# Optimization experiments

Hardware: AMD Instinct MI355X
Metric: run time of the kernel (lower is better)

The kernel has to match this reference:

```python
import jax, jax.numpy as jnp
import numpy as np
import math

B, INST, C, HEADS, DH, CTX = 1, 4, 320, 8, 40, 768
FULL, HW = 512, 4096
SCALE = DH ** -0.5
EPS = 1e-5


def _ln(x, g, b):
    m = x.mean(-1, keepdims=True)
    v = ((x - m) ** 2).mean(-1, keepdims=True)
    return (x - m) / jnp.sqrt(v + EPS) * g + b


def _mha(x, ctx, Wq, Wk, Wv, Wo, bo, mask=None):
    # x: [b, n, C]; ctx: [b, m, ctx_dim]; mask: [b, n, m] bool (True = keep)
    b, n, _ = x.shape
    m = ctx.shape[1]
    q = (x @ Wq).reshape(b, n, HEADS, DH)
    k = (ctx @ Wk).reshape(b, m, HEADS, DH)
    v = (ctx @ Wv).reshape(b, m, HEADS, DH)
    sim = jnp.einsum('bihd,bjhd->bhij', q, k) * SCALE
    if mask is not None:
        sim = jnp.where(mask[:, None, :, :], sim, -jnp.finfo(sim.dtype).max)
    attn = jax.nn.softmax(sim, axis=-1)
    out = jnp.einsum('bhij,bjhd->bihd', attn, v).reshape(b, n, HEADS * DH)
    return out @ Wo + bo


def _fourier(x, num_freqs=8, temperature=100.0):
    freqs = temperature ** (jnp.arange(num_freqs, dtype=x.dtype) / num_freqs)
    parts = []
    for i in range(num_freqs):
        parts.append(jnp.sin(freqs[i] * x))
        parts.append(jnp.cos(freqs[i] * x))
    return jax.lax.stop_gradient(jnp.concatenate(parts, axis=-1))  # @torch.no_grad in source


def _resize(x, H, W):
    # torch F.interpolate bilinear, align_corners=False (half-pixel), no antialias
    return jax.image.resize(x, x.shape[:2] + (H, W), method='bilinear', antialias=False)


def setup_inputs() -> dict:
    key = jax.random.key(0)
    ks = jax.random.split(key, 32)
    s = 0.02
    inp = {
        'ca_x': jax.random.normal(ks[0], (B, INST + 1, HW, C), jnp.float32),
        'guidance_mask': jax.random.uniform(ks[1], (B, INST, FULL, FULL), jnp.float32),
        'supplement_mask': jax.random.uniform(ks[2], (B, 1, FULL, FULL), jnp.float32),
        'image_token': jax.random.normal(ks[3], (B, INST + 1, HW, C), jnp.float32),
        'context': jax.random.normal(ks[4], (INST + 1, 77, CTX), jnp.float32),
        'box': jax.random.uniform(ks[5], (B, INST, 8), jnp.float32),
        'img_features': jax.random.normal(ks[6], (B * INST, 257, CTX), jnp.float32),
        'bg_features': jax.random.normal(ks[7], (B, 257, CTX), jnp.float32),
        'sigmoid_values': jax.random.uniform(ks[8], (B, INST, FULL, FULL), jnp.float32),
        'Wq_obj': jax.random.normal(ks[9], (C, C), jnp.float32) * s,
        'Wk_obj': jax.random.normal(ks[10], (CTX, C), jnp.float32) * s,
        'Wv_obj': jax.random.normal(ks[11], (CTX, C), jnp.float32) * s,
        'Wo_obj': jax.random.normal(ks[12], (C, C), jnp.float32) * s,
        'bo_obj': jnp.zeros((C,), jnp.float32),
        'ln_g_obj': jnp.ones((C,), jnp.float32),
        'ln_b_obj': jnp.zeros((C,), jnp.float32),
        'Wq2': jax.random.normal(ks[13], (C, C), jnp.float32) * s,
        'Wk2': jax.random.normal(ks[14], (CTX, C), jnp.float32) * s,
        'Wv2': jax.random.normal(ks[15], (CTX, C), jnp.float32) * s,
        'Wo2': jax.random.normal(ks[16], (C, C), jnp.float32) * s,
        'bo2': jnp.zeros((C,), jnp.float32),
        'ln_g2': jnp.ones((C,), jnp.float32),
        'ln_b2': jnp.zeros((C,), jnp.float32),
        'pn_W1': jax.random.normal(ks[17], (128, 512), jnp.float32) * s,
        'pn_b1': jnp.zeros((512,), jnp.float32),
        'pn_W2': jax.random.normal(ks[18], (512, 512), jnp.float32) * s,
        'pn_b2': jnp.zeros((512,), jnp.float32),
        'pn_W3': jax.random.normal(ks[19], (512, CTX), jnp.float32) * s,
        'pn_b3': jnp.zeros((CTX,), jnp.float32),
        'la_Wq': jax.random.normal(ks[20], (C, C), jnp.float32) * s,
        'la_Wk': jax.random.normal(ks[21], (C, C), jnp.float32) * s,
        'la_Wv': jax.random.normal(ks[22], (C, C), jnp.float32) * s,
        'la_Wo': jax.random.normal(ks[23], (C, C), jnp.float32) * s,
        'la_bo': jnp.zeros((C,), jnp.float32),
        'height': FULL,
        'width': FULL,
    }
    return inp


def reference(ca_x, guidance_mask, supplement_mask, image_token, context, box,
              img_features, bg_features, sigmoid_values,
              Wq_obj, Wk_obj, Wv_obj, Wo_obj, bo_obj, ln_g_obj, ln_b_obj,
              Wq2, Wk2, Wv2, Wo2, bo2, ln_g2, ln_b2,
              pn_W1, pn_b1, pn_W2, pn_b2, pn_W3, pn_b3,
              la_Wq, la_Wk, la_Wv, la_Wo, la_bo,
              height, width):
    b, _, hw, c = ca_x.shape
    inst = guidance_mask.shape[1]
    down = int(math.sqrt(height * width // hw))
    H, W = height // down, width // down

    gm = _resize(guidance_mask, H, W)           # [B, inst, H, W]
    supp = _resize(supplement_mask, H, W)       # [B, 1, H, W]
    sig = _resize(sigmoid_values, H, W).reshape(b, inst, hw, 1)

    # PositionNet on boxes
    box_emb = _fourier(box.reshape(b * inst, 1, 8))          # [B*inst, 1, 128]
    h1 = jax.nn.silu(box_emb @ pn_W1 + pn_b1)
    h2 = jax.nn.silu(h1 @ pn_W2 + pn_b2)
    box_token = h2 @ pn_W3 + pn_b3                            # [B*inst, 1, 768]

    # foreground cross-attention (ea_obj)
    context_fg = jnp.concatenate([context[1:], img_features, box_token], axis=1)
    q_in = _ln(image_token[:, 1:].reshape(b * inst, hw, c), ln_g_obj, ln_b_obj)
    ea_x = _mha(q_in, context_fg, Wq_obj, Wk_obj, Wv_obj, Wo_obj, bo_obj)
    ea_x = ea_x.reshape(b, inst, hw, c) * sig

    ca_inst = ca_x[:, 1:] * sig + ea_x                        # [B, inst, HW, C]

    # background cross-attention (ea2)
    context_bg = jnp.concatenate([context[0:1], bg_features], axis=1)
    q2 = _ln(ca_inst.sum(axis=1).reshape(b, hw, c), ln_g2, ln_b2)
    ea_bg = _mha(q2, context_bg, Wq2, Wk2, Wv2, Wo2, bo2)     # [B, HW, C]
    ca0 = ca_x[:, 0] + ea_bg

    # layout self-attention with guidance-mask sparsity
    gm_all = jnp.concatenate([gm, supp], axis=1).reshape(b, inst + 1, hw)
    # sum over phases of outer products; clamp-to-1 in source only feeds the ==0 test
    sim_mask = jnp.einsum('bpi,bpj->bij', gm_all, gm_all) != 0  # [B, HW, HW] keep-mask
    fusion = _mha(image_token[:, 0], image_token[:, 0],
                  la_Wq, la_Wk, la_Wv, la_Wo, la_bo, mask=sim_mask)

    out = ca0 + ca_inst.sum(axis=1) + fusion                  # [B, HW, C]
    return out
```

## Files before the change

### kernel.cpp

```cpp
#include <hip/hip_runtime.h>
#include <hip/hip_bf16.h>
#include <math.h>

typedef unsigned short bhalf;
typedef unsigned int u32;
typedef unsigned long long u64;
typedef __attribute__((ext_vector_type(8))) short s16x8;
typedef __attribute__((ext_vector_type(4))) float f32x4;

#define SCALE_QK 0.15811388300841898f
#define K2E (SCALE_QK * 1.4426950408889634f)
#define NEG_INF (-3.402823466e38f)

__device__ __forceinline__ float bf2f(bhalf u){
    union { unsigned int i; float f; } v; v.i = ((unsigned int)u) << 16; return v.f;
}
__device__ __forceinline__ bhalf f2bf(float f){
    unsigned int x = __float_as_uint(f);
    unsigned int r = (x + 0x7fffu + ((x >> 16) & 1u)) >> 16;
    return (bhalf)r;
}
__device__ __forceinline__ float fexp2(float x){
    float r; asm("v_exp_f32 %0, %1" : "=v"(r) : "v"(x)); return r;
}
__device__ __forceinline__ u32 cvtpk(float lo, float hi){
    u32 r; asm("v_cvt_pk_bf16_f32 %0, %1, %2" : "=v"(r) : "v"(lo), "v"(hi)); return r;
}

struct WT12 { const float* in[12]; bhalf* out[12]; };

struct PrepArgs {
    const float *itok, *g_obj, *b_obj; bhalf *q_in, *x_la;
    WT12 wt;
    const float *gmask, *smask, *sgv; float *gm_all, *sig;
    const float *box, *W1, *b1, *W2, *b2, *W3, *b3; float* tok;
};

__global__ __launch_bounds__(320) void mega_prep(PrepArgs a){
    __shared__ float smem[64 * 65];
    const int bid = blockIdx.x, tid = threadIdx.x;
    if (bid < 16){
        float* emb = smem; float* h1 = smem + 128; float* h2 = smem + 640;
        const int bb = bid >> 2, sl = bid & 3;
        for (int t = tid; t < 128; t += 320){
            const int i = t >> 4, jj = t & 15, j = jj & 7;
            const float f = powf(100.f, (float)i * 0.125f);
            const float v = f * a.box[bb * 8 + j];
            emb[t] = (jj < 8) ? sinf(v) : cosf(v);
        }
        __syncthreads();
        for (int t = tid; t < 512; t += 320){
            float a0 = a.b1[t], a1 = 0.f, a2 = 0.f, a3 = 0.f;
#pragma unroll 8
            for (int k = 0; k < 32; ++k){
                a0 += emb[k]      * a.W1[k * 512 + t];
                a1 += emb[k + 32] * a.W1[(k + 32) * 512 + t];
                a2 += emb[k + 64] * a.W1[(k + 64) * 512 + t];
                a3 += emb[k + 96] * a.W1[(k + 96) * 512 + t];
            }
            const float x = (a0 + a1) + (a2 + a3);
            h1[t] = x / (1.f + __expf(-x));
        }
        __syncthreads();
        for (int t = tid; t < 512; t += 320){
            float a0 = a.b2[t], a1 = 0.f, a2 = 0.f, a3 = 0.f;
#pragma unroll 8
            for (int k = 0; k < 128; ++k){
                a0 += h1[k]       * a.W2[k * 512 + t];
                a1 += h1[k + 128] * a.W2[(k + 128) * 512 + t];
                a2 += h1[k + 256] * a.W2[(k + 256) * 512 + t];
                a3 += h1[k + 384] * a.W2[(k + 384) * 512 + t];
            }
            const float x = (a0 + a1) + (a2 + a3);
            h2[t] = x / (1.f + __expf(-x));
        }
        __syncthreads();
        if (tid < 192){
            const int t = sl * 192 + tid;
            float a0 = a.b3[t], a1 = 0.f, a2 = 0.f, a3 = 0.f;
#pragma unroll 8
            for (int k = 0; k < 128; ++k){
                a0 += h2[k]       * a.W3[k * 768 + t];
                a1 += h2[k + 128] * a.W3[(k + 128) * 768 + t];
                a2 += h2[k + 256] * a.W3[(k + 256) * 768 + t];
                a3 += h2[k + 384] * a.W3[(k + 384) * 768 + t];
            }
            a.tok[bb * 768 + t] = (a0 + a1) + (a2 + a3);
        }
    } else if (bid < 456){
        float (*T)[65] = (float(*)[65])smem;
        const int b = bid - 16;
        int w, t, K;
        if (b < 200){ w = b / 25; t = b % 25; K = 320; }
        else        { w = 8 + (b - 200) / 60; t = (b - 200) % 60; K = 768; }
        const int k0 = (t / 5) * 64, n0 = (t % 5) * 64;
        const float* in = a.wt.in[w];
        bhalf* out = a.wt.out[w];
        const int c = tid & 63, wv = tid >> 6;
        if (tid < 256){
#pragma unroll
            for (int r = 0; r < 16; ++r)
                T[wv + r * 4][c] = in[(long)(k0 + wv + r * 4) * 320 + n0 + c];
        }
        __syncthreads();
        if (tid < 256){
#pragma unroll
            for (int r = 0; r < 16; ++r)
                out[(long)(n0 + wv + r * 4) * K + k0 + c] = f2bf(T[c][wv + r * 4]);
        }
    } else if (bid < 600){
        if (tid < 256){
            const int b = bid - 456;
            const int p = b >> 4;
            const int i = (b & 15) * 256 + tid;
            const int y = i >> 6, x = i & 63;
            const int o = (8 * y + 3) * 512 + 8 * x + 3;
            const float* s; float* dst;
            if (p < 4){ s = a.gmask + (long)p * 262144; dst = a.gm_all + p * 4096; }
            else if (p == 4){ s = a.smask; dst = a.gm_all + 4 * 4096; }
            else { s = a.sgv + (long)(p - 5) * 262144; dst = a.sig + (p - 5) * 4096; }
            dst[i] = 0.25f * (s[o] + s[o + 1] + s[o + 512] + s[o + 513]);
        }
    } else {
        const int lane = tid & 63, wv = tid >> 6;
        const int wgid = (bid - 600) * 5 + wv;
        for (int row = wgid; row < 20480; row += 10240){
            if (row >= 16384){
                const int rr = row - 16384;
#pragma unroll
                for (int j = 0; j < 5; ++j){
                    const int c = lane + 64 * j;
                    a.x_la[(long)rr * 320 + c] = f2bf(a.itok[(long)rr * 320 + c]);
                }
                continue;
            }
            float v[5];
            float s = 0.f, sq = 0.f;
#pragma unroll
            for (int j = 0; j < 5; ++j){
                v[j] = a.itok[(long)(4096 + row) * 320 + lane + 64 * j];
                s += v[j]; sq += v[j] * v[j];
            }
#pragma unroll
            for (int o = 1; o < 64; o <<= 1){ s += __shfl_xor(s, o); sq += __shfl_xor(sq, o); }
            const float mean = s * (1.f / 320.f);
            const float var  = sq * (1.f / 320.f) - mean * mean;
            const float inv  = rsqrtf(var + 1e-5f);
#pragma unroll
            for (int j = 0; j < 5; ++j){
                const int c = lane + 64 * j;
                a.q_in[(long)row * 320 + c] = f2bf((v[j] - mean) * inv * a.g_obj[c] + a.b_obj[c]);
            }
        }
    }
}

__global__ __launch_bounds__(256) void mega_mask(
    const float* __restrict__ gm_all, u64* __restrict__ mb,
    const float* __restrict__ context, const float* __restrict__ imgf,
    const float* __restrict__ bgf, const float* __restrict__ boxtok, bhalf* __restrict__ out)
{
    __shared__ float smem[5440];
    const int tid = threadIdx.x;
    if (blockIdx.x < 256){
        const int r = blockIdx.x;
        const int i0 = (r & 63) << 6, j0 = (r >> 6) << 10;
        float* gi = smem;
        float* gj = smem + 320;
        for (int idx = tid; idx < 5 * 64; idx += 256)
            gi[idx] = gm_all[(idx >> 6) * 4096 + i0 + (idx & 63)];
        for (int idx = tid; idx < 5 * 1024; idx += 256)
            gj[idx] = gm_all[(idx >> 10) * 4096 + j0 + (idx & 1023)];
        __syncthreads();
        const int lane = tid & 63, wave = tid >> 6;
        const float a0 = gi[lane], a1 = gi[64 + lane], a2 = gi[128 + lane],
                    a3 = gi[192 + lane], a4 = gi[256 + lane];
        for (int ww = wave; ww < 16; ww += 4){
            u64 m = 0;
            for (int j = 0; j < 64; ++j){
                const int jj = (ww << 6) + j;
                const float dot = a0 * gj[jj] + a1 * gj[1024 + jj] + a2 * gj[2048 + jj]
                                + a3 * gj[3072 + jj] + a4 * gj[4096 + jj];
                m |= (u64)(dot != 0.f) << j;
            }
            mb[(long)((j0 >> 6) + ww) * 4096 + (i0 + lane)] = m;
        }
    } else {
        const int idx = (blockIdx.x - 256) * 256 + tid;
        const int i = idx / (336 * 768);
        const int r = (idx / 768) % 336;
        const int c = idx % 768;
        float v;
        if (i < 4){
            if (r < 77)       v = context[((long)(1 + i) * 77 + r) * 768 + c];
            else if (r < 334) v = imgf[((long)i * 257 + (r - 77)) * 768 + c];
            else if (r == 334) v = boxtok[i * 768 + c];
            else v = 0.f;
        } else {
            if (r < 77)       v = context[(long)r * 768 + c];
            else if (r < 334) v = bgf[(long)(r - 77) * 768 + c];
            else v = 0.f;
        }
        out[idx] = f2bf(v);
    }
}

template<int K>
__device__ __forceinline__ void gemm5x4_body(
    int bx, int by, const bhalf* __restrict__ A, const bhalf* __restrict__ Wt,
    bhalf* __restrict__ Cbf, int M, int kdm, float scale)
{
    const int wave = threadIdx.x >> 6, lane = threadIdx.x & 63;
    const int mb = bx * 256 + wave * 64;
    const int n0 = by * 64;
    const int klo = (lane >> 4) * 8;
    const bhalf* ap[4];
#pragma unroll
    for (int f = 0; f < 4; ++f){
        int mrow = mb + f * 16 + (lane & 15); if (mrow > M - 1) mrow = M - 1;
        ap[f] = A + (long)mrow * K + klo;
    }
    const bhalf* wp = Wt + (long)(n0 + (lane & 15)) * K + klo;
    const f32x4 fz = {0.f, 0.f, 0.f, 0.f};
    f32x4 acc[4][4];
#pragma unroll
    for (int f = 0; f < 4; ++f)
#pragma unroll
        for (int t = 0; t < 4; ++t) acc[f][t] = fz;
#pragma unroll
    for (int k0 = 0; k0 < K; k0 += 32){
        s16x8 av[4];
#pragma unroll
        for (int f = 0; f < 4; ++f) av[f] = *(const s16x8*)(ap[f] + k0);
        s16x8 bv[4];
#pragma unroll
        for (int t = 0; t < 4; ++t) bv[t] = *(const s16x8*)(wp + (long)t * 16 * K + k0);
#pragma unroll
        for (int f = 0; f < 4; ++f)
#pragma unroll
            for (int t = 0; t < 4; ++t)
                acc[f][t] = __builtin_amdgcn_mfma_f32_16x16x32_bf16(av[f], bv[t], acc[f][t], 0, 0, 0);
    }
#pragma unroll
    for (int f = 0; f < 4; ++f){
        const int rb = mb + f * 16 + ((threadIdx.x & 63) >> 4) * 4;
#pragma unroll
        for (int t = 0; t < 4; ++t){
            const int col = n0 + t * 16 + (threadIdx.x & 15);
            const int hh = col / 40, cc = col % 40;
#pragma unroll
            for (int r = 0; r < 4; ++r){
                const int row = rb + r;
                if (row >= M) continue;
                Cbf[(((long)(row / kdm) * 8 + hh) * kdm + (row % kdm)) * 40 + cc] = f2bf(acc[f][t][r] * scale);
            }
        }
    }
}

template<int K>
__device__ __forceinline__ void gemm_vt_body(
    int bx, int by, const bhalf* __restrict__ A, const bhalf* __restrict__ Wt,
    bhalf* __restrict__ Vt, int M, int vt_ns, int PAD, bhalf (*Tsh)[72])
{
    const int wave = threadIdx.x >> 6, lane = threadIdx.x & 63;
    const int m0 = bx * 64 + wave * 16;
    const int n0 = by * 64;
    int mrow = m0 + (lane & 15); if (mrow > M - 1) mrow = M - 1;
    const int klo = (lane >> 4) * 8;
    const bhalf* ap = A + (long)mrow * K + klo;
    const bhalf* wp = Wt + (long)(n0 + (lane & 15)) * K + klo;
    const f32x4 fz = {0.f, 0.f, 0.f, 0.f};
    f32x4 acc[4]; acc[0] = fz; acc[1] = fz; acc[2] = fz; acc[3] = fz;
#pragma unroll
    for (int k0 = 0; k0 < K; k0 += 32){
        s16x8 a = *(const s16x8*)(ap + k0);
#pragma unroll
        for (int t = 0; t < 4; ++t){
            s16x8 b = *(const s16x8*)(wp + (long)t * 16 * K + k0);
            acc[t] = __builtin_amdgcn_mfma_f32_16x16x32_bf16(a, b, acc[t], 0, 0, 0);
        }
    }
    const int hi = lane >> 4, l15 = lane & 15;
#pragma unroll
    for (int t = 0; t < 4; ++t)
#pragma unroll
        for (int r = 0; r < 4; ++r)
            Tsh[wave * 16 + hi * 4 + r][t * 16 + l15] = f2bf(acc[t][r]);
    __syncthreads();
    const int c = threadIdx.x & 63, jq = threadIdx.x >> 6;
    const int jbase = bx * 64 + jq * 16;
    if (jbase >= PAD) return;
    bhalf* vp = Vt + (long)(n0 + c) * vt_ns + jbase;
    if (jbase + 16 <= M){
        u32 wb[8];
#pragma unroll
        for (int p = 0; p < 8; ++p)
            wb[p] = (u32)Tsh[jq * 16 + 2 * p][c] | ((u32)Tsh[jq * 16 + 2 * p + 1][c] << 16);
        *(uint4*)vp       = make_uint4(wb[0], wb[1], wb[2], wb[3]);
        *(uint4*)(vp + 8) = make_uint4(wb[4], wb[5], wb[6], wb[7]);
    } else if (jbase >= M){
        *(uint4*)vp       = make_uint4(0, 0, 0, 0);
        *(uint4*)(vp + 8) = make_uint4(0, 0, 0, 0);
    } else {
        for (int jj = 0; jj < 16; ++jj)
            vp[jj] = (jbase + jj < M) ? Tsh[jq * 16 + jj][c] : (bhalf)0;
    }
}

struct ProjArgs {
    const bhalf *q_in, *ctx_all, *x_la;
    const bhalf *wqobjT, *wkobjT, *wk2T, *lawqT, *wvobjT, *wv2T, *lawvT;
    bhalf *q_obj, *k_obj, *k_bg, *qkl, *vt_obj, *vt_bg, *vt_l;
};

__global__ __launch_bounds__(256) void proj_packed(ProjArgs a){
    const int r = blockIdx.x;
    if (r < 320)       gemm5x4_body<320>(r % 64, r / 64, a.q_in, a.wqobjT, a.q_obj, 16384, 4096, K2E);
    else if (r < 480){ const int s = r - 320; const int by = s / 16, bx = s % 16;
        gemm5x4_body<320>(bx, by, a.x_la, a.lawqT, a.qkl, 4096, 4096, by < 5 ? K2E : 1.f); }
    else if (r < 510){ const int s = r - 480; gemm5x4_body<768>(s % 6, s / 6, a.ctx_all, a.wkobjT, a.k_obj, 1344, 336, 1.f); }
    else { const int s = r - 510; gemm5x4_body<768>(s % 2, s / 2, a.ctx_all + (size_t)4 * 336 * 768, a.wk2T, a.k_bg, 336, 336, 1.f); }
}

__global__ __launch_bounds__(256) void proj_vt(ProjArgs a){
    __shared__ bhalf Tsh[64][72];
    const int r = blockIdx.x;
    if (r < 150){ const int bz = r / 30, rem = r % 30;
        if (bz == 4) gemm_vt_body<768>(rem % 6, rem / 6, a.ctx_all + (size_t)4 * 336 * 768, a.wv2T, a.vt_bg, 336, 384, 384, Tsh);
        else gemm_vt_body<768>(rem % 6, rem / 6, a.ctx_all + (size_t)bz * 336 * 768, a.wvobjT, a.vt_obj + (size_t)bz * 320 * 384, 336, 384, 384, Tsh);
    }
    else { const int s = r - 150; gemm_vt_body<320>(s % 64, s / 64, a.x_la, a.lawvT, a.vt_l, 4096, 4096, 4096, Tsh); }
}

__global__ __launch_bounds__(256) void ln_rows_kernel(
    const float* __restrict__ in, const float* __restrict__ g, const float* __restrict__ b,
    bhalf* __restrict__ out)
{
    const int lane = threadIdx.x & 63;
    const int wgid = blockIdx.x * 4 + (threadIdx.x >> 6);
    for (int row = wgid; row < 4096; row += 4096){
        float v[5];
        float s = 0.f, sq = 0.f;
#pragma unroll
        for (int j = 0; j < 5; ++j){
            v[j] = in[(long)row * 320 + lane + 64 * j];
            s += v[j]; sq += v[j] * v[j];
        }
#pragma unroll
        for (int o = 1; o < 64; o <<= 1){ s += __shfl_xor(s, o); sq += __shfl_xor(sq, o); }
        const float mean = s * (1.f / 320.f);
        const float var  = sq * (1.f / 320.f) - mean * mean;
        const float inv  = rsqrtf(var + 1e-5f);
#pragma unroll
        for (int j = 0; j < 5; ++j){
            const int c = lane + 64 * j;
            out[(long)row * 320 + c] = f2bf((v[j] - mean) * inv * g[c] + b[c]);
        }
    }
}

template<int MODE>
__global__ __launch_bounds__(256) void gemm320(
    const bhalf* __restrict__ A, const bhalf* __restrict__ Wt,
    const float* __restrict__ bias, bhalf* __restrict__ Cbf,
    float* __restrict__ Cf, const float* __restrict__ add1, const float* __restrict__ add2,
    int M, int kdm, float ascale,
    const bhalf* __restrict__ A2, const bhalf* __restrict__ Wt2, const float* __restrict__ bias2)
{
    constexpr int K = 320;
    const int wave = threadIdx.x >> 6, lane = threadIdx.x & 63;
    const int m0 = blockIdx.x * 64 + wave * 16;
    const int n0 = blockIdx.y * 64;
    int mrow = m0 + (lane & 15); if (mrow > M - 1) mrow = M - 1;
    const int klo = (lane >> 4) * 8;
    const bhalf* ap = A + (long)mrow * K + klo;
    const bhalf* wp = Wt + (long)(n0 + (lane & 15)) * K + klo;
    const f32x4 fz = {0.f, 0.f, 0.f, 0.f};
    f32x4 acc[4]; acc[0] = fz; acc[1] = fz; acc[2] = fz; acc[3] = fz;
#pragma unroll
    for (int k0 = 0; k0 < K; k0 += 32){
        s16x8 a = *(const s16x8*)(ap + k0);
#pragma unroll
        for (int t = 0; t < 4; ++t){
            s16x8 b = *(const s16x8*)(wp + (long)t * 16 * K + k0);
            acc[t] = __builtin_amdgcn_mfma_f32_16x16x32_bf16(a, b, acc[t], 0, 0, 0);
        }
    }
    if (MODE == 6){
        const bhalf* ap2 = A2 + (long)mrow * K + klo;
        const bhalf* wp2 = Wt2 + (long)(n0 + (lane & 15)) * K + klo;
#pragma unroll
        for (int k0 = 0; k0 < K; k0 += 32){
            s16x8 a = *(const s16x8*)(ap2 + k0);
#pragma unroll
            for (int t = 0; t < 4; ++t){
                s16x8 b = *(const s16x8*)(wp2 + (long)t * 16 * K + k0);
                acc[t] = __builtin_amdgcn_mfma_f32_16x16x32_bf16(a, b, acc[t], 0, 0, 0);
            }
        }
    }
    if (MODE == 8){
#pragma unroll
        for (int i = 1; i < 4; ++i){
            const bhalf* api = A + (long)i * kdm + (long)mrow * K + klo;
#pragma unroll
            for (int k0 = 0; k0 < K; k0 += 32){
                s16x8 a = *(const s16x8*)(api + k0);
#pragma unroll
                for (int t = 0; t < 4; ++t){
                    s16x8 b = *(const s16x8*)(wp + (long)t * 16 * K + k0);
                    acc[t] = __builtin_amdgcn_mfma_f32_16x16x32_bf16(a, b, acc[t], 0, 0, 0);
                }
            }
        }
    }
    const int rb = m0 + (lane >> 4) * 4;
    int rin[4], rn[4];
    if (MODE == 5){
#pragma unroll
        for (int r = 0; r < 4; ++r){ const int row = rb + r; rin[r] = row / kdm; rn[r] = row % kdm; }
    }
#pragma unroll
    for (int t = 0; t < 4; ++t){
        const int col = n0 + t * 16 + (lane & 15);
        const int hh = col / 40, cc = col % 40;
#pragma unroll
        for (int r = 0; r < 4; ++r){
            const int row = rb + r;
            if (row >= M) continue;
            const float v = acc[t][r];
            if (MODE == 5)
                Cbf[(((long)rin[r] * 8 + hh) * kdm + rn[r]) * 40 + cc] = f2bf(v * ascale);
            else if (MODE == 6){
                const long o = (long)row * 320 + col;
                Cf[o] = v + bias[col] + bias2[col] + add1[o] + add2[o];
            }
            else if (MODE == 8){
                const long o = (long)row * 320 + col;
                float ssum = 0.f, cax = 0.f;
#pragma unroll
                for (int i = 0; i < 4; ++i){
                    const float sg = add2[i * 4096 + row];
                    ssum += sg;
                    cax += sg * add1[(long)i * 4096 * 320 + o];
                }
                Cf[o] = v + ssum * bias[col] + cax;
            }
        }
    }
}

template<bool GMM, bool PARTIAL, bool SIG>
__global__ __launch_bounds__(256) void flash4(
    const bhalf* __restrict__ Qh, const bhalf* __restrict__ Kh, const bhalf* __restrict__ Vt,
    bhalf* __restrict__ O, const u64* __restrict__ maskb,
    int NKV, long qh_is, long qh_hs, long kh_is, long kh_hs, long vt_is, int vt_ns, long o_is,
    const float* __restrict__ sigp, bhalf* __restrict__ pacc, float* __restrict__ pl)
{
    const int lane = threadIdx.x & 63, wave = threadIdx.x >> 6;
    const int l15 = lane & 15, hi = lane >> 4, klo = hi * 8;
    const int h = blockIdx.y;
    const int inst = PARTIAL ? 0 : blockIdx.z;
    const int g = PARTIAL ? blockIdx.z : 0;
    const int qbase = blockIdx.x * 256 + wave * 64;
    const s16x8 z8 = {0, 0, 0, 0, 0, 0, 0, 0};
    const f32x4 fz = {0.f, 0.f, 0.f, 0.f};

    s16x8 qa0[4], qa1[4];
#pragma unroll
    for (int qg = 0; qg < 4; ++qg){
        const bhalf* qp = Qh + inst * qh_is + h * qh_hs + (long)(qbase + qg * 16 + l15) * 40;
        qa0[qg] = *(const s16x8*)(qp + klo);
        qa1[qg] = (hi == 0) ? *(const s16x8*)(qp + 32) : z8;
    }
    const int krbase = 8 * (l15 >> 2) + (l15 & 3);
    const bhalf* khead = Kh + inst * kh_is + h * kh_hs;
    const bhalf* kbase = khead + (long)krbase * 40;

    const bhalf* vbase[3];
#pragma unroll
    for (int ct = 0; ct < 3; ++ct){
        int dr = h * 40 + ct * 16 + l15; if (dr > 319) dr = 319;
        vbase[ct] = Vt + inst * vt_is + (long)dr * vt_ns + hi * 8;
    }

    f32x4 acc[4][3];
    float l_run[4];
#pragma unroll
    for (int qg = 0; qg < 4; ++qg){
        acc[qg][0] = fz; acc[qg][1] = fz; acc[qg][2] = fz;
        l_run[qg] = 0.f;
    }

    auto soft_pv = [&](f32x4 (&d)[4], s16x8 (&vb)[3][2], float& lr, f32x4 (&ac)[3]){
        float csum = 0.f;
#pragma unroll
        for (int t = 0; t < 4; ++t)
#pragma unroll
            for (int r = 0; r < 4; ++r){
                const float p = fexp2(d[t][r]);
                d[t][r] = p; csum += p;
            }
        csum += __shfl_xor(csum, 16);
        csum += __shfl_xor(csum, 32);
        lr += csum;
#pragma unroll
        for (int s = 0; s < 2; ++s){
            union { u32 w[4]; s16x8 v; } pb;
            pb.w[0] = cvtpk(d[2 * s][0], d[2 * s][1]);
            pb.w[1] = cvtpk(d[2 * s][2], d[2 * s][3]);
            pb.w[2] = cvtpk(d[2 * s + 1][0], d[2 * s + 1][1]);
            pb.w[3] = cvtpk(d[2 * s + 1][2], d[2 * s + 1][3]);
#pragma unroll
            for (int ct = 0; ct < 3; ++ct)
                ac[ct] = __builtin_amdgcn_mfma_f32_16x16x32_bf16(vb[ct][s], pb.v, ac[ct], 0, 0, 0);
        }
    };

    const int ch0 = PARTIAL ? g * 8 : 0;
    const int chN = PARTIAL ? ch0 + 8 : (NKV >> 6);
    for (int ch = ch0; ch < chN; ++ch){
        const int c0 = ch << 6;
        s16x8 k0[4], k1[4];
#pragma unroll
        for (int t = 0; t < 4; ++t){
            const int toff = ((t >> 1) << 5) + ((t & 1) << 2);
            const bhalf* kp = kbase + (long)(c0 + toff) * 40;
            k0[t] = *(const s16x8*)(kp + klo);
            k1[t] = (hi == 0) ? *(const s16x8*)(kp + 32) : z8;
        }
        s16x8 vb[3][2];
#pragma unroll
        for (int ct = 0; ct < 3; ++ct)
#pragma unroll
            for (int s = 0; s < 2; ++s)
                vb[ct][s] = *(const s16x8*)(vbase[ct] + c0 + 32 * s);
        u64 M[4];
        if (GMM){
#pragma unroll
            for (int qg = 0; qg < 4; ++qg)
                M[qg] = maskb[(long)ch * 4096 + qbase + qg * 16 + l15];
        }
#pragma unroll
        for (int qg = 0; qg < 4; ++qg){
            f32x4 d[4];
#pragma unroll
            for (int t = 0; t < 4; ++t){
                d[t] = __builtin_amdgcn_mfma_f32_16x16x32_bf16(k0[t], qa0[qg], fz, 0, 0, 0);
                d[t] = __builtin_amdgcn_mfma_f32_16x16x32_bf16(k1[t], qa1[qg], d[t], 0, 0, 0);
            }
            if (GMM && !__all(M[qg] == ~0ull)){
                const u64 Mh = M[qg] >> (hi * 8);
#pragma unroll
                for (int t = 0; t < 4; ++t){
                    const int tb = ((t >> 1) << 5) + ((t & 1) << 2);
#pragma unroll
                    for (int r = 0; r < 4; ++r)
                        if (!((Mh >> (tb + r)) & 1)) d[t][r] = NEG_INF;
                }
            }
            soft_pv(d, vb, l_run[qg], acc[qg]);
        }
    }
    if (!PARTIAL && (NKV & 63)){
        const int c0 = (NKV >> 6) << 6;
        s16x8 k0[4], k1[4];
#pragma unroll
        for (int t = 0; t < 4; ++t){
            const int toff = ((t >> 1) << 5) + ((t & 1) << 2);
            int kr = c0 + toff + krbase; if (kr > NKV - 1) kr = NKV - 1;
            const bhalf* kp = khead + (long)kr * 40;
            k0[t] = *(const s16x8*)(kp + klo);
            k1[t] = (hi == 0) ? *(const s16x8*)(kp + 32) : z8;
        }
        s16x8 vb[3][2];
#pragma unroll
        for (int ct = 0; ct < 3; ++ct)
#pragma unroll
            for (int s = 0; s < 2; ++s)
                vb[ct][s] = *(const s16x8*)(vbase[ct] + c0 + 32 * s);
#pragma unroll
        for (int qg = 0; qg < 4; ++qg){
            f32x4 d[4];
#pragma unroll
            for (int t = 0; t < 4; ++t){
                d[t] = __builtin_amdgcn_mfma_f32_16x16x32_bf16(k0[t], qa0[qg], fz, 0, 0, 0);
                d[t] = __builtin_amdgcn_mfma_f32_16x16x32_bf16(k1[t], qa1[qg], d[t], 0, 0, 0);
            }
#pragma unroll
            for (int t = 0; t < 4; ++t){
                const int tb = ((t >> 1) << 5) + ((t & 1) << 2);
#pragma unroll
                for (int r = 0; r < 4; ++r)
                    if (c0 + tb + hi * 8 + r >= NKV) d[t][r] = NEG_INF;
            }
            soft_pv(d, vb, l_run[qg], acc[qg]);
        }
    }

    if (PARTIAL){
#pragma unroll
        for (int qg = 0; qg < 4; ++qg){
            const int q = qbase + qg * 16 + l15;
#pragma unroll
            for (int ct = 0; ct < 3; ++ct){
                bhalf* pb = pacc + ((((size_t)(g * 8 + h) * 3 + ct) * 4 + hi) * 4096 + q) * 4;
                uint2 w;
                w.x = cvtpk(acc[qg][ct][0], acc[qg][ct][1]);
                w.y = cvtpk(acc[qg][ct][2], acc[qg][ct][3]);
                *(uint2*)pb = w;
            }
            if (hi == 0)
                pl[(size_t)(g * 8 + h) * 4096 + q] = l_run[qg];
        }
    } else {
#pragma unroll
        for (int qg = 0; qg < 4; ++qg){
            const int q = qbase + qg * 16 + l15;
            float sc = 1.f / l_run[qg];
            if (SIG) sc *= sigp[(long)inst * 4096 + q];
            bhalf* op = O + inst * o_is + (long)q * 320 + h * 40;
#pragma unroll
            for (int ct = 0; ct < 3; ++ct){
                const int d0 = ct * 16 + hi * 4;
                if (d0 < 40){
                    uint2 w;
                    w.x = cvtpk(acc[qg][ct][0] * sc, acc[qg][ct][1] * sc);
                    w.y = cvtpk(acc[qg][ct][2] * sc, acc[qg][ct][3] * sc);
                    *(uint2*)(op + d0) = w;
                }
            }
        }
    }
}

__global__ __launch_bounds__(256) void combine_kernel(
    const bhalf* __restrict__ pacc, const float* __restrict__ pl, bhalf* __restrict__ O)
{
    const int idx = blockIdx.x * 256 + threadIdx.x;
    const int h = idx / (3 * 4096);
    const int r2 = idx % (3 * 4096);
    const int ct = r2 >> 12, q = r2 & 4095;
    float ls = 0.f;
#pragma unroll
    for (int g = 0; g < 8; ++g) ls += pl[(size_t)(g * 8 + h) * 4096 + q];
    float acc[16];
#pragma unroll
    for (int d = 0; d < 16; ++d) acc[d] = 0.f;
#pragma unroll
    for (int g = 0; g < 8; ++g){
#pragma unroll
        for (int hi = 0; hi < 4; ++hi){
            const ushort4 v = *(const ushort4*)(pacc + ((((size_t)(g * 8 + h) * 3 + ct) * 4 + hi) * 4096 + q) * 4);
            acc[hi * 4 + 0] += bf2f(v.x);
            acc[hi * 4 + 1] += bf2f(v.y);
            acc[hi * 4 + 2] += bf2f(v.z);
            acc[hi * 4 + 3] += bf2f(v.w);
        }
    }
    const float inv = 1.f / ls;
    bhalf* op = O + (size_t)q * 320 + h * 40 + ct * 16;
    if (ct < 2){
        u32 wb[8];
#pragma unroll
        for (int d = 0; d < 8; ++d) wb[d] = cvtpk(acc[2 * d] * inv, acc[2 * d + 1] * inv);
        *(uint4*)op       = make_uint4(wb[0], wb[1], wb[2], wb[3]);
        *(uint4*)(op + 8) = make_uint4(wb[4], wb[5], wb[6], wb[7]);
    } else {
        u32 wb[4];
#pragma unroll
        for (int d = 0; d < 4; ++d) wb[d] = cvtpk(acc[2 * d] * inv, acc[2 * d + 1] * inv);
        *(uint4*)op = make_uint4(wb[0], wb[1], wb[2], wb[3]);
    }
}

extern "C" void kernel_launch(void* const* d_in, const int* in_sizes, int n_in,
                              void* d_out, int out_size, void* d_ws, size_t ws_size,
                              hipStream_t stream)
{
    (void)in_sizes; (void)n_in; (void)out_size; (void)ws_size;
    const float* ca_x   = (const float*)d_in[0];
    const float* gmask  = (const float*)d_in[1];
    const float* smask  = (const float*)d_in[2];
    const float* itok   = (const float*)d_in[3];
    const float* ctx    = (const float*)d_in[4];
    const float* box    = (const float*)d_in[5];
    const float* imgf   = (const float*)d_in[6];
    const float* bgf    = (const float*)d_in[7];
    const float* sgv    = (const float*)d_in[8];
    const float* Wq_obj = (const float*)d_in[9];
    const float* Wk_obj = (const float*)d_in[10];
    const float* Wv_obj = (const float*)d_in[11];
    const float* Wo_obj = (const float*)d_in[12];
    const float* bo_obj = (const float*)d_in[13];
    const float* g_obj  = (const float*)d_in[14];
    const float* b_obj  = (const float*)d_in[15];
    const float* Wq2    = (const float*)d_in[16];
    const float* Wk2    = (const float*)d_in[17];
    const float* Wv2    = (const float*)d_in[18];
    const float* Wo2    = (const float*)d_in[19];
    const float* bo2    = (const float*)d_in[20];
    const float* g2     = (const float*)d_in[21];
    const float* b2     = (const float*)d_in[22];
    const float* pnW1   = (const float*)d_in[23];
    const float* pnb1   = (const float*)d_in[24];
    const float* pnW2   = (const float*)d_in[25];
    const float* pnb2   = (const float*)d_in[26];
    const float* pnW3   = (const float*)d_in[27];
    const float* pnb3   = (const float*)d_in[28];
    const float* laWq   = (const float*)d_in[29];
    const float* laWk   = (const float*)d_in[30];
    const float* laWv   = (const float*)d_in[31];
    const float* laWo   = (const float*)d_in[32];
    const float* labo   = (const float*)d_in[33];

    char* wsp = (char*)d_ws; size_t off = 0;
    auto alloc = [&](size_t bytes) -> void* {
        void* p = wsp + off; off += (bytes + 255) & ~(size_t)255; return p;
    };
    bhalf* wqobjT = (bhalf*)alloc(320 * 320 * 2);
    bhalf* woobjT = (bhalf*)alloc(320 * 320 * 2);
    bhalf* wq2T   = (bhalf*)alloc(320 * 320 * 2);
    bhalf* wo2T   = (bhalf*)alloc(320 * 320 * 2);
    bhalf* lawqT  = (bhalf*)alloc(320 * 320 * 2);
    bhalf* lawkT  = (bhalf*)alloc(320 * 320 * 2);
    bhalf* lawvT  = (bhalf*)alloc(320 * 320 * 2);
    bhalf* lawoT  = (bhalf*)alloc(320 * 320 * 2);
    bhalf* wkobjT = (bhalf*)alloc(768 * 320 * 2);
    bhalf* wvobjT = (bhalf*)alloc(768 * 320 * 2);
    bhalf* wk2T   = (bhalf*)alloc(768 * 320 * 2);
    bhalf* wv2T   = (bhalf*)alloc(768 * 320 * 2);
    float* gm_all = (float*)alloc(5 * 4096 * 4);
    float* sig    = (float*)alloc(4 * 4096 * 4);
    float* boxtok = (float*)alloc(4 * 768 * 4);
    u64*   maskb  = (u64*)alloc((size_t)64 * 4096 * 8);
    bhalf* ctx_all= (bhalf*)alloc((size_t)5 * 336 * 768 * 2);
    bhalf* q_in   = (bhalf*)alloc((size_t)16384 * 320 * 2);
    bhalf* x_la   = (bhalf*)alloc((size_t)4096 * 320 * 2);
    bhalf* k_obj  = (bhalf*)alloc((size_t)4 * 336 * 320 * 2);
    bhalf* vt_obj = (bhalf*)alloc((size_t)4 * 320 * 384 * 2);
    bhalf* k_bg   = (bhalf*)alloc((size_t)336 * 320 * 2);
    bhalf* vt_bg  = (bhalf*)alloc((size_t)320 * 384 * 2);
    bhalf* q_obj  = (bhalf*)alloc((size_t)16384 * 320 * 2);
    bhalf* o_obj  = (bhalf*)alloc((size_t)16384 * 320 * 2);
    float* Sbuf   = (float*)alloc((size_t)4096 * 320 * 4);
    bhalf* q2v    = (bhalf*)alloc((size_t)4096 * 320 * 2);
    bhalf* q2p    = (bhalf*)alloc((size_t)4096 * 320 * 2);
    bhalf* o2     = (bhalf*)alloc((size_t)4096 * 320 * 2);
    bhalf* qkl    = (bhalf*)alloc((size_t)2 * 4096 * 320 * 2);
    bhalf* vt_l   = (bhalf*)alloc((size_t)320 * 4096 * 2);
    bhalf* ol     = (bhalf*)alloc((size_t)4096 * 320 * 2);

    bhalf* pacc = (bhalf*)q_in;
    float* pl   = (float*)(pacc + (size_t)8 * 8 * 3 * 4 * 4096 * 4);

    PrepArgs pa{};
    pa.itok = itok; pa.g_obj = g_obj; pa.b_obj = b_obj; pa.q_in = q_in; pa.x_la = x_la;
    pa.wt.in[0] = Wq_obj; pa.wt.out[0] = wqobjT;
    pa.wt.in[1] = Wo_obj; pa.wt.out[1] = woobjT;
    pa.wt.in[2] = Wq2;    pa.wt.out[2] = wq2T;
    pa.wt.in[3] = Wo2;    pa.wt.out[3] = wo2T;
    pa.wt.in[4] = laWq;   pa.wt.out[4] = lawqT;
    pa.wt.in[5] = laWk;   pa.wt.out[5] = lawkT;
    pa.wt.in[6] = laWv;   pa.wt.out[6] = lawvT;
    pa.wt.in[7] = laWo;   pa.wt.out[7] = lawoT;
    pa.wt.in[8] = Wk_obj; pa.wt.out[8] = wkobjT;
    pa.wt.in[9] = Wv_obj; pa.wt.out[9] = wvobjT;
    pa.wt.in[10] = Wk2;   pa.wt.out[10] = wk2T;
    pa.wt.in[11] = Wv2;   pa.wt.out[11] = wv2T;
    pa.gmask = gmask; pa.smask = smask; pa.sgv = sgv; pa.gm_all = gm_all; pa.sig = sig;
    pa.box = box; pa.W1 = pnW1; pa.b1 = pnb1; pa.W2 = pnW2; pa.b2 = pnb2; pa.W3 = pnW3; pa.b3 = pnb3;
    pa.tok = boxtok;
    mega_prep<<<dim3(2648), 320, 0, stream>>>(pa);

    mega_mask<<<dim3(5296), 256, 0, stream>>>(gm_all, maskb, ctx, imgf, bgf, boxtok, ctx_all);

    ProjArgs pj{};
    pj.q_in = q_in; pj.ctx_all = ctx_all; pj.x_la = x_la;
    pj.wqobjT = wqobjT; pj.wkobjT = wkobjT; pj.wk2T = wk2T; pj.lawqT = lawqT;
    pj.wvobjT = wvobjT; pj.wv2T = wv2T; pj.lawvT = lawvT;
    pj.q_obj = q_obj; pj.k_obj = k_obj; pj.k_bg = k_bg; pj.qkl = qkl;
    pj.vt_obj = vt_obj; pj.vt_bg = vt_bg; pj.vt_l = vt_l;
    proj_packed<<<dim3(520), 256, 0, stream>>>(pj);
    proj_vt<<<dim3(470), 256, 0, stream>>>(pj);

    flash4<false, false, true><<<dim3(16, 8, 4), 256, 0, stream>>>(q_obj, k_obj, vt_obj, o_obj, nullptr,
        335, (long)8 * 4096 * 40, (long)4096 * 40, (long)8 * 336 * 40, (long)336 * 40,
        (long)320 * 384, 384, (long)4096 * 320, sig, nullptr, nullptr);

    gemm320<8><<<dim3(64, 5), 256, 0, stream>>>(o_obj, woobjT, bo_obj, nullptr, Sbuf,
        ca_x + (size_t)4096 * 320, sig, 4096, 4096 * 320, 1.f, nullptr, nullptr, nullptr);

    ln_rows_kernel<<<dim3(1024), 256, 0, stream>>>(Sbuf, g2, b2, q2v);

    gemm320<5><<<dim3(64, 5), 256, 0, stream>>>(q2v, wq2T, nullptr, q2p, nullptr, nullptr, nullptr,
        4096, 4096, K2E, nullptr, nullptr, nullptr);

    flash4<false, false, false><<<dim3(16, 8, 1), 256, 0, stream>>>(q2p, k_bg, vt_bg, o2, nullptr,
        334, 0, (long)4096 * 40, 0, (long)336 * 40, 0, 384, 0, nullptr, nullptr, nullptr);

    flash4<true, true, false><<<dim3(16, 8, 8), 256, 0, stream>>>(qkl, qkl + (size_t)8 * 4096 * 40, vt_l, nullptr, maskb,
        4096, 0, (long)4096 * 40, 0, (long)4096 * 40, 0, 4096, 0, nullptr, pacc, pl);

    combine_kernel<<<dim3(384), 256, 0, stream>>>(pacc, pl, ol);

    gemm320<6><<<dim3(64, 5), 256, 0, stream>>>(o2, wo2T, bo2, nullptr, (float*)d_out, ca_x, Sbuf,
        4096, 1, 1.f, ol, lawoT, labo);
}
```

Measured before the change: 321.6 us.

## Fold q/x_la projections into mask kernel; stage MLP weights in LDS

Moves the Q-object, layout QK and layout V projections, which depend only on prep outputs, into the mega_mask launch as extra blocks. The context K/V projections stay in a smaller proj_ctx kernel, which removes one launch and lets the independent GEMMs overlap the mask and context-conversion work. The box-token MLP in mega_prep now stages weight chunks into shared memory with float4 loads instead of strided global reads. The cost is a larger LDS footprint in mega_prep and more per-block branching in mega_mask, which may lower occupancy.

```diff
diff --git a/kernel.cpp b/kernel.cpp
--- a/kernel.cpp
+++ b/kernel.cpp
@@ -28,6 +28,115 @@
 }
 
 struct WT12 { const float* in[12]; bhalf* out[12]; };
+
+struct ProjArgs {
+    const bhalf *q_in, *ctx_all, *x_la;
+    const bhalf *wqobjT, *wkobjT, *wk2T, *lawqT, *wvobjT, *wv2T, *lawvT;
+    bhalf *q_obj, *k_obj, *k_bg, *qkl, *vt_obj, *vt_bg, *vt_l;
+};
+
+template<int K>
+__device__ __forceinline__ void gemm5x4_body(
+    int bx, int by, const bhalf* __restrict__ A, const bhalf* __restrict__ Wt,
+    bhalf* __restrict__ Cbf, int M, int kdm, float scale)
+{
+    const int wave = threadIdx.x >> 6, lane = threadIdx.x & 63;
+    const int mb = bx * 256 + wave * 64;
+    const int n0 = by * 64;
+    const int klo = (lane >> 4) * 8;
+    const bhalf* ap[4];
+#pragma unroll
+    for (int f = 0; f < 4; ++f){
+        int mrow = mb + f * 16 + (lane & 15); if (mrow > M - 1) mrow = M - 1;
+        ap[f] = A + (long)mrow * K + klo;
+    }
+    const bhalf* wp = Wt + (long)(n0 + (lane & 15)) * K + klo;
+    const f32x4 fz = {0.f, 0.f, 0.f, 0.f};
+    f32x4 acc[4][4];
+#pragma unroll
+    for (int f = 0; f < 4; ++f)
+#pragma unroll
+        for (int t = 0; t < 4; ++t) acc[f][t] = fz;
+#pragma unroll
+    for (int k0 = 0; k0 < K; k0 += 32){
+        s16x8 av[4];
+#pragma unroll
+        for (int f = 0; f < 4; ++f) av[f] = *(const s16x8*)(ap[f] + k0);
+        s16x8 bv[4];
+#pragma unroll
+        for (int t = 0; t < 4; ++t) bv[t] = *(const s16x8*)(wp + (long)t * 16 * K + k0);
+#pragma unroll
+        for (int f = 0; f < 4; ++f)
+#pragma unroll
+            for (int t = 0; t < 4; ++t)
+                acc[f][t] = __builtin_amdgcn_mfma_f32_16x16x32_bf16(av[f], bv[t], acc[f][t], 0, 0, 0);
+    }
+#pragma unroll
+    for (int f = 0; f < 4; ++f){
+        const int rb = mb + f * 16 + ((threadIdx.x & 63) >> 4) * 4;
+#pragma unroll
+        for (int t = 0; t < 4; ++t){
+            const int col = n0 + t * 16 + (threadIdx.x & 15);
+            const int hh = col / 40, cc = col % 40;
+#pragma unroll
+            for (int r = 0; r < 4; ++r){
+                const int row = rb + r;
+                if (row >= M) continue;
+                Cbf[(((long)(row / kdm) * 8 + hh) * kdm + (row % kdm)) * 40 + cc] = f2bf(acc[f][t][r] * scale);
+            }
+        }
+    }
+}
+
+template<int K>
+__device__ __forceinline__ void gemm_vt_body(
+    int bx, int by, const bhalf* __restrict__ A, const bhalf* __restrict__ Wt,
+    bhalf* __restrict__ Vt, int M, int vt_ns, int PAD, bhalf (*Tsh)[72])
+{
+    const int wave = threadIdx.x >> 6, lane = threadIdx.x & 63;
+    const int m0 = bx * 64 + wave * 16;
+    const int n0 = by * 64;
+    int mrow = m0 + (lane & 15); if (mrow > M - 1) mrow = M - 1;
+    const int klo = (lane >> 4) * 8;
+    const bhalf* ap = A + (long)mrow * K + klo;
+    const bhalf* wp = Wt + (long)(n0 + (lane & 15)) * K + klo;
+    const f32x4 fz = {0.f, 0.f, 0.f, 0.f};
+    f32x4 acc[4]; acc[0] = fz; acc[1] = fz; acc[2] = fz; acc[3] = fz;
+#pragma unroll
+    for (int k0 = 0; k0 < K; k0 += 32){
+        s16x8 a = *(const s16x8*)(ap + k0);
+#pragma unroll
+        for (int t = 0; t < 4; ++t){
+            s16x8 b = *(const s16x8*)(wp + (long)t * 16 * K + k0);
+            acc[t] = __builtin_amdgcn_mfma_f32_16x16x32_bf16(a, b, acc[t], 0, 0, 0);
+        }
+    }
+    const int hi = lane >> 4, l15 = lane & 15;
+#pragma unroll
+    for (int t = 0; t < 4; ++t)
+#pragma unroll
+        for (int r = 0; r < 4; ++r)
+            Tsh[wave * 16 + hi * 4 + r][t * 16 + l15] = f2bf(acc[t][r]);
+    __syncthreads();
+    const int c = threadIdx.x & 63, jq = threadIdx.x >> 6;
+    const int jbase = bx * 64 + jq * 16;
+    if (jbase >= PAD) return;
+    bhalf* vp = Vt + (long)(n0 + c) * vt_ns + jbase;
+    if (jbase + 16 <= M){
+        u32 wb[8];
+#pragma unroll
+        for (int p = 0; p < 8; ++p)
+            wb[p] = (u32)Tsh[jq * 16 + 2 * p][c] | ((u32)Tsh[jq * 16 + 2 * p + 1][c] << 16);
+        *(uint4*)vp       = make_uint4(wb[0], wb[1], wb[2], wb[3]);
+        *(uint4*)(vp + 8) = make_uint4(wb[4], wb[5], wb[6], wb[7]);
+    } else if (jbase >= M){
+        *(uint4*)vp       = make_uint4(0, 0, 0, 0);
+        *(uint4*)(vp + 8) = make_uint4(0, 0, 0, 0);
+    } else {
+        for (int jj = 0; jj < 16; ++jj)
+            vp[jj] = (jbase + jj < M) ? Tsh[jq * 16 + jj][c] : (bhalf)0;
+    }
+}
 
 struct PrepArgs {
     const float *itok, *g_obj, *b_obj; bhalf *q_in, *x_la;
@@ -37,10 +146,14 @@
 };
 
 __global__ __launch_bounds__(320) void mega_prep(PrepArgs a){
-    __shared__ float smem[64 * 65];
+    __shared__ float smem[9344];
     const int bid = blockIdx.x, tid = threadIdx.x;
     if (bid < 16){
-        float* emb = smem; float* h1 = smem + 128; float* h2 = smem + 640;
+        float* emb = smem;
+        float* h1  = smem + 128;
+        float* h2  = smem + 640;
+        float* WS  = smem + 1152;
+        float4* WS4 = (float4*)WS;
         const int bb = bid >> 2, sl = bid & 3;
         for (int t = tid; t < 128; t += 320){
             const int i = t >> 4, jj = t & 15, j = jj & 7;
@@ -49,43 +162,60 @@
             emb[t] = (jj < 8) ? sinf(v) : cosf(v);
         }
         __syncthreads();
-        for (int t = tid; t < 512; t += 320){
-            float a0 = a.b1[t], a1 = 0.f, a2 = 0.f, a3 = 0.f;
-#pragma unroll 8
-            for (int k = 0; k < 32; ++k){
-                a0 += emb[k]      * a.W1[k * 512 + t];
-                a1 += emb[k + 32] * a.W1[(k + 32) * 512 + t];
-                a2 += emb[k + 64] * a.W1[(k + 64) * 512 + t];
-                a3 += emb[k + 96] * a.W1[(k + 96) * 512 + t];
-            }
-            const float x = (a0 + a1) + (a2 + a3);
-            h1[t] = x / (1.f + __expf(-x));
+        {
+            float a0 = a.b1[tid];
+            float a1 = (tid < 192) ? a.b1[320 + tid] : 0.f;
+            for (int c0 = 0; c0 < 128; c0 += 16){
+                const float4* src = (const float4*)(a.W1 + (long)c0 * 512);
+                for (int idx = tid; idx < 2048; idx += 320) WS4[idx] = src[idx];
+                __syncthreads();
+#pragma unroll
+                for (int k = 0; k < 16; ++k){
+                    const float e = emb[c0 + k];
+                    a0 += WS[k * 512 + tid] * e;
+                    if (tid < 192) a1 += WS[k * 512 + 320 + tid] * e;
+                }
+                __syncthreads();
+            }
+            h1[tid] = a0 / (1.f + __expf(-a0));
+            if (tid < 192) h1[320 + tid] = a1 / (1.f + __expf(-a1));
         }
         __syncthreads();
-        for (int t = tid; t < 512; t += 320){
-            float a0 = a.b2[t], a1 = 0.f, a2 = 0.f, a3 = 0.f;
-#pragma unroll 8
-            for (int k = 0; k < 128; ++k){
-                a0 += h1[k]       * a.W2[k * 512 + t];
-                a1 += h1[k + 128] * a.W2[(k + 128) * 512 + t];
-                a2 += h1[k + 256] * a.W2[(k + 256) * 512 + t];
-                a3 += h1[k + 384] * a.W2[(k + 384) * 512 + t];
-            }
-            const float x = (a0 + a1) + (a2 + a3);
-            h2[t] = x / (1.f + __expf(-x));
+        {
+            float a0 = a.b2[tid];
+            float a1 = (tid < 192) ? a.b2[320 + tid] : 0.f;
+            for (int c0 = 0; c0 < 512; c0 += 16){
+                const float4* src = (const float4*)(a.W2 + (long)c0 * 512);
+                for (int idx = tid; idx < 2048; idx += 320) WS4[idx] = src[idx];
+                __syncthreads();
+#pragma unroll
+                for (int k = 0; k < 16; ++k){
+                    const float e = h1[c0 + k];
+                    a0 += WS[k * 512 + tid] * e;
+                    if (tid < 192) a1 += WS[k * 512 + 320 + tid] * e;
+                }
+                __syncthreads();
+            }
+            h2[tid] = a0 / (1.f + __expf(-a0));
+            if (tid < 192) h2[320 + tid] = a1 / (1.f + __expf(-a1));
         }
         __syncthreads();
-        if (tid < 192){
-            const int t = sl * 192 + tid;
-            float a0 = a.b3[t], a1 = 0.f, a2 = 0.f, a3 = 0.f;
-#pragma unroll 8
-            for (int k = 0; k < 128; ++k){
-                a0 += h2[k]       * a.W3[k * 768 + t];
-                a1 += h2[k + 128] * a.W3[(k + 128) * 768 + t];
-                a2 += h2[k + 256] * a.W3[(k + 256) * 768 + t];
-                a3 += h2[k + 384] * a.W3[(k + 384) * 768 + t];
-            }
-            a.tok[bb * 768 + t] = (a0 + a1) + (a2 + a3);
+        {
+            float a0 = (tid < 192) ? a.b3[sl * 192 + tid] : 0.f;
+            for (int c0 = 0; c0 < 512; c0 += 16){
+                for (int idx = tid; idx < 768; idx += 320){
+                    const int rr = idx / 48, cc = idx % 48;
+                    WS4[rr * 48 + cc] = *(const float4*)(a.W3 + (long)(c0 + rr) * 768 + sl * 192 + cc * 4);
+                }
+                __syncthreads();
+                if (tid < 192){
+#pragma unroll
+                    for (int k = 0; k < 16; ++k)
+                        a0 += WS[k * 192 + tid] * h2[c0 + k];
+                }
+                __syncthreads();
+            }
+            if (tid < 192) a.tok[bb * 768 + sl * 192 + tid] = a0;
         }
     } else if (bid < 456){
         float (*T)[65] = (float(*)[65])smem;
@@ -158,12 +288,13 @@
 __global__ __launch_bounds__(256) void mega_mask(
     const float* __restrict__ gm_all, u64* __restrict__ mb,
     const float* __restrict__ context, const float* __restrict__ imgf,
-    const float* __restrict__ bgf, const float* __restrict__ boxtok, bhalf* __restrict__ out)
+    const float* __restrict__ bgf, const float* __restrict__ boxtok, bhalf* __restrict__ out,
+    ProjArgs a)
 {
     __shared__ float smem[5440];
     const int tid = threadIdx.x;
-    if (blockIdx.x < 256){
-        const int r = blockIdx.x;
+    const int r = blockIdx.x;
+    if (r < 256){
         const int i0 = (r & 63) << 6, j0 = (r >> 6) << 10;
         float* gi = smem;
         float* gj = smem + 320;
@@ -185,152 +316,45 @@
             }
             mb[(long)((j0 >> 6) + ww) * 4096 + (i0 + lane)] = m;
         }
-    } else {
-        const int idx = (blockIdx.x - 256) * 256 + tid;
+    } else if (r < 5296){
+        const int idx = (r - 256) * 256 + tid;
         const int i = idx / (336 * 768);
-        const int r = (idx / 768) % 336;
+        const int rr = (idx / 768) % 336;
         const int c = idx % 768;
         float v;
         if (i < 4){
-            if (r < 77)       v = context[((long)(1 + i) * 77 + r) * 768 + c];
-            else if (r < 334) v = imgf[((long)i * 257 + (r - 77)) * 768 + c];
-            else if (r == 334) v = boxtok[i * 768 + c];
+            if (rr < 77)       v = context[((long)(1 + i) * 77 + rr) * 768 + c];
+            else if (rr < 334) v = imgf[((long)i * 257 + (rr - 77)) * 768 + c];
+            else if (rr == 334) v = boxtok[i * 768 + c];
             else v = 0.f;
         } else {
-            if (r < 77)       v = context[(long)r * 768 + c];
-            else if (r < 334) v = bgf[(long)(r - 77) * 768 + c];
+            if (rr < 77)       v = context[(long)rr * 768 + c];
+            else if (rr < 334) v = bgf[(long)(rr - 77) * 768 + c];
             else v = 0.f;
         }
         out[idx] = f2bf(v);
-    }
-}
-
-template<int K>
-__device__ __forceinline__ void gemm5x4_body(
-    int bx, int by, const bhalf* __restrict__ A, const bhalf* __restrict__ Wt,
-    bhalf* __restrict__ Cbf, int M, int kdm, float scale)
-{
-    const int wave = threadIdx.x >> 6, lane = threadIdx.x & 63;
-    const int mb = bx * 256 + wave * 64;
-    const int n0 = by * 64;
-    const int klo = (lane >> 4) * 8;
-    const bhalf* ap[4];
-#pragma unroll
-    for (int f = 0; f < 4; ++f){
-        int mrow = mb + f * 16 + (lane & 15); if (mrow > M - 1) mrow = M - 1;
-        ap[f] = A + (long)mrow * K + klo;
-    }
-    const bhalf* wp = Wt + (long)(n0 + (lane & 15)) * K + klo;
-    const f32x4 fz = {0.f, 0.f, 0.f, 0.f};
-    f32x4 acc[4][4];
-#pragma unroll
-    for (int f = 0; f < 4; ++f)
-#pragma unroll
-        for (int t = 0; t < 4; ++t) acc[f][t] = fz;
-#pragma unroll
-    for (int k0 = 0; k0 < K; k0 += 32){
-        s16x8 av[4];
-#pragma unroll
-        for (int f = 0; f < 4; ++f) av[f] = *(const s16x8*)(ap[f] + k0);
-        s16x8 bv[4];
-#pragma unroll
-        for (int t = 0; t < 4; ++t) bv[t] = *(const s16x8*)(wp + (long)t * 16 * K + k0);
-#pragma unroll
-        for (int f = 0; f < 4; ++f)
-#pragma unroll
-            for (int t = 0; t < 4; ++t)
-                acc[f][t] = __builtin_amdgcn_mfma_f32_16x16x32_bf16(av[f], bv[t], acc[f][t], 0, 0, 0);
-    }
-#pragma unroll
-    for (int f = 0; f < 4; ++f){
-        const int rb = mb + f * 16 + ((threadIdx.x & 63) >> 4) * 4;
-#pragma unroll
-        for (int t = 0; t < 4; ++t){
-            const int col = n0 + t * 16 + (threadIdx.x & 15);
-            const int hh = col / 40, cc = col % 40;
-#pragma unroll
-            for (int r = 0; r < 4; ++r){
-                const int row = rb + r;
-                if (row >= M) continue;
-                Cbf[(((long)(row / kdm) * 8 + hh) * kdm + (row % kdm)) * 40 + cc] = f2bf(acc[f][t][r] * scale);
-            }
-        }
-    }
-}
-
-template<int K>
-__device__ __forceinline__ void gemm_vt_body(
-    int bx, int by, const bhalf* __restrict__ A, const bhalf* __restrict__ Wt,
-    bhalf* __restrict__ Vt, int M, int vt_ns, int PAD, bhalf (*Tsh)[72])
-{
-    const int wave = threadIdx.x >> 6, lane = threadIdx.x & 63;
-    const int m0 = bx * 64 + wave * 16;
-    const int n0 = by * 64;
-    int mrow = m0 + (lane & 15); if (mrow > M - 1) mrow = M - 1;
-    const int klo = (lane >> 4) * 8;
-    const bhalf* ap = A + (long)mrow * K + klo;
-    const bhalf* wp = Wt + (long)(n0 + (lane & 15)) * K + klo;
-    const f32x4 fz = {0.f, 0.f, 0.f, 0.f};
-    f32x4 acc[4]; acc[0] = fz; acc[1] = fz; acc[2] = fz; acc[3] = fz;
-#pragma unroll
-    for (int k0 = 0; k0 < K; k0 += 32){
-        s16x8 a = *(const s16x8*)(ap + k0);
-#pragma unroll
-        for (int t = 0; t < 4; ++t){
-            s16x8 b = *(const s16x8*)(wp + (long)t * 16 * K + k0);
-            acc[t] = __builtin_amdgcn_mfma_f32_16x16x32_bf16(a, b, acc[t], 0, 0, 0);
-        }
-    }
-    const int hi = lane >> 4, l15 = lane & 15;
-#pragma unroll
-    for (int t = 0; t < 4; ++t)
-#pragma unroll
-        for (int r = 0; r < 4; ++r)
-            Tsh[wave * 16 + hi * 4 + r][t * 16 + l15] = f2bf(acc[t][r]);
-    __syncthreads();
-    const int c = threadIdx.x & 63, jq = threadIdx.x >> 6;
-    const int jbase = bx * 64 + jq * 16;
-    if (jbase >= PAD) return;
-    bhalf* vp = Vt + (long)(n0 + c) * vt_ns + jbase;
-    if (jbase + 16 <= M){
-        u32 wb[8];
-#pragma unroll
-        for (int p = 0; p < 8; ++p)
-            wb[p] = (u32)Tsh[jq * 16 + 2 * p][c] | ((u32)Tsh[jq * 16 + 2 * p + 1][c] << 16);
-        *(uint4*)vp       = make_uint4(wb[0], wb[1], wb[2], wb[3]);
-        *(uint4*)(vp + 8) = make_uint4(wb[4], wb[5], wb[6], wb[7]);
-    } else if (jbase >= M){
-        *(uint4*)vp       = make_uint4(0, 0, 0, 0);
-        *(uint4*)(vp + 8) = make_uint4(0, 0, 0, 0);
+    } else if (r < 5616){
+        const int s = r - 5296;
+        gemm5x4_body<320>(s % 64, s / 64, a.q_in, a.wqobjT, a.q_obj, 16384, 4096, K2E);
+    } else if (r < 5776){
+        const int s = r - 5616; const int by = s / 16, bx = s % 16;
+        gemm5x4_body<320>(bx, by, a.x_la, a.lawqT, a.qkl, 4096, 4096, by < 5 ? K2E : 1.f);
     } else {
-        for (int jj = 0; jj < 16; ++jj)
-            vp[jj] = (jbase + jj < M) ? Tsh[jq * 16 + jj][c] : (bhalf)0;
-    }
-}
-
-struct ProjArgs {
-    const bhalf *q_in, *ctx_all, *x_la;
-    const bhalf *wqobjT, *wkobjT, *wk2T, *lawqT, *wvobjT, *wv2T, *lawvT;
-    bhalf *q_obj, *k_obj, *k_bg, *qkl, *vt_obj, *vt_bg, *vt_l;
-};
-
-__global__ __launch_bounds__(256) void proj_packed(ProjArgs a){
-    const int r = blockIdx.x;
-    if (r < 320)       gemm5x4_body<320>(r % 64, r / 64, a.q_in, a.wqobjT, a.q_obj, 16384, 4096, K2E);
-    else if (r < 480){ const int s = r - 320; const int by = s / 16, bx = s % 16;
-        gemm5x4_body<320>(bx, by, a.x_la, a.lawqT, a.qkl, 4096, 4096, by < 5 ? K2E : 1.f); }
-    else if (r < 510){ const int s = r - 480; gemm5x4_body<768>(s % 6, s / 6, a.ctx_all, a.wkobjT, a.k_obj, 1344, 336, 1.f); }
-    else { const int s = r - 510; gemm5x4_body<768>(s % 2, s / 2, a.ctx_all + (size_t)4 * 336 * 768, a.wk2T, a.k_bg, 336, 336, 1.f); }
-}
-
-__global__ __launch_bounds__(256) void proj_vt(ProjArgs a){
+        const int s = r - 5776;
+        bhalf (*Tsh)[72] = (bhalf(*)[72])smem;
+        gemm_vt_body<320>(s % 64, s / 64, a.x_la, a.lawvT, a.vt_l, 4096, 4096, 4096, Tsh);
+    }
+}
+
+__global__ __launch_bounds__(256) void proj_ctx(ProjArgs a){
     __shared__ bhalf Tsh[64][72];
     const int r = blockIdx.x;
-    if (r < 150){ const int bz = r / 30, rem = r % 30;
+    if (r < 30)       gemm5x4_body<768>(r % 6, r / 6, a.ctx_all, a.wkobjT, a.k_obj, 1344, 336, 1.f);
+    else if (r < 40){ const int s = r - 30; gemm5x4_body<768>(s % 2, s / 2, a.ctx_all + (size_t)4 * 336 * 768, a.wk2T, a.k_bg, 336, 336, 1.f); }
+    else { const int s = r - 40; const int bz = s / 30, rem = s % 30;
         if (bz == 4) gemm_vt_body<768>(rem % 6, rem / 6, a.ctx_all + (size_t)4 * 336 * 768, a.wv2T, a.vt_bg, 336, 384, 384, Tsh);
         else gemm_vt_body<768>(rem % 6, rem / 6, a.ctx_all + (size_t)bz * 336 * 768, a.wvobjT, a.vt_obj + (size_t)bz * 320 * 384, 336, 384, 384, Tsh);
     }
-    else { const int s = r - 150; gemm_vt_body<320>(s % 64, s / 64, a.x_la, a.lawvT, a.vt_l, 4096, 4096, 4096, Tsh); }
 }
 
 __global__ __launch_bounds__(256) void ln_rows_kernel(
@@ -774,16 +798,16 @@
     pa.tok = boxtok;
     mega_prep<<<dim3(2648), 320, 0, stream>>>(pa);
 
-    mega_mask<<<dim3(5296), 256, 0, stream>>>(gm_all, maskb, ctx, imgf, bgf, boxtok, ctx_all);
-
     ProjArgs pj{};
     pj.q_in = q_in; pj.ctx_all = ctx_all; pj.x_la = x_la;
     pj.wqobjT = wqobjT; pj.wkobjT = wkobjT; pj.wk2T = wk2T; pj.lawqT = lawqT;
     pj.wvobjT = wvobjT; pj.wv2T = wv2T; pj.lawvT = lawvT;
     pj.q_obj = q_obj; pj.k_obj = k_obj; pj.k_bg = k_bg; pj.qkl = qkl;
     pj.vt_obj = vt_obj; pj.vt_bg = vt_bg; pj.vt_l = vt_l;
-    proj_packed<<<dim3(520), 256, 0, stream>>>(pj);
-    proj_vt<<<dim3(470), 256, 0, stream>>>(pj);
+
+    mega_mask<<<dim3(6096), 256, 0, stream>>>(gm_all, maskb, ctx, imgf, bgf, boxtok, ctx_all, pj);
+
+    proj_ctx<<<dim3(190), 256, 0, stream>>>(pj);
 
     flash4<false, false, true><<<dim3(16, 8, 4), 256, 0, stream>>>(q_obj, k_obj, vt_obj, o_obj, nullptr,
         335, (long)8 * 4096 * 40, (long)4096 * 40, (long)8 * 336 * 40, (long)336 * 40,
```

Result: slower. 406.5 us (+26.4%).
